# Optimization experiments

Measured on AMD Instinct MI355X. Metric: run time of the kernel, lower is better.

Reference implementation:

```python
import jax, jax.numpy as jnp
import numpy as np

DIM = 1024
HEADS = 16
DIM_HEAD = 64
B = 16
N = 512
INNER = HEADS * DIM_HEAD            # 1024
CPB_DIM = DIM // 2                  # 512
INNER_FF = int(DIM * 4 * 2 / 3)     # 2730
EPS = 1e-5


def setup_inputs() -> dict:
    key = jax.random.key(0)
    ks = jax.random.split(key, 10)
    s = lambda i, shape, scale: jax.random.normal(ks[i], shape, jnp.float32) * scale
    return dict(
        x=s(0, (B, N, DIM), 1.0),
        g_ln=jnp.ones((DIM,), jnp.float32),
        Wq=s(1, (DIM, INNER), 0.02),
        Wkv=s(2, (DIM, 2 * INNER), 0.02),
        Wo=s(3, (INNER, DIM), 0.02),
        cpb_w1=s(4, (1, CPB_DIM), 0.5),
        cpb_b1=jnp.zeros((CPB_DIM,), jnp.float32),
        cpb_w2=s(5, (CPB_DIM, CPB_DIM), 0.05),
        cpb_b2=jnp.zeros((CPB_DIM,), jnp.float32),
        cpb_w3=s(6, (CPB_DIM, HEADS), 0.05),
        cpb_b3=jnp.zeros((HEADS,), jnp.float32),
        ff_w_in=s(7, (2 * INNER_FF, DIM), 0.02),
        ff_g=jnp.ones((INNER_FF,), jnp.float32),
        ff_w_out=s(8, (DIM, INNER_FF), 0.02),
    )


def _seq_ln(x, g):
    # Faithful to repo's LayerNorm: mean/var over dim=1 (sequence axis of [b,n,d])
    mean = jnp.mean(x, axis=1, keepdims=True)
    var = jnp.var(x, axis=1, keepdims=True)  # unbiased=False
    return (x - mean) * jax.lax.rsqrt(jnp.maximum(var, EPS)) * g


def reference(x, g_ln, Wq, Wkv, Wo, cpb_w1, cpb_b1, cpb_w2, cpb_b2, cpb_w3, cpb_b3,
              ff_w_in, ff_g, ff_w_out):
    b, n, d = x.shape
    # ContinuousPositionBias (1D, 2 layers)
    pos = jnp.arange(n, dtype=jnp.float32)
    rel = (pos[:, None] - pos[None, :])[..., None]           # [n,n,1]
    rel = jnp.sign(rel) * jnp.log(jnp.abs(rel) + 1.0)        # log-distance
    h = jax.nn.silu(rel @ cpb_w1 + cpb_b1)
    h = jax.nn.silu(h @ cpb_w2 + cpb_b2)
    bias = (h @ cpb_w3 + cpb_b3).transpose(2, 0, 1)          # [h,n,n]

    # Attention (framerate=None -> no pos_embeds; context = x)
    xn = _seq_ln(x, g_ln)
    q = xn @ Wq
    k, v = jnp.split(xn @ Wkv, 2, axis=-1)
    to_heads = lambda t: t.reshape(b, n, HEADS, DIM_HEAD).transpose(0, 2, 1, 3)
    q, k, v = to_heads(q), to_heads(k), to_heads(v)
    q = q * (DIM_HEAD ** -0.5)
    sim = jnp.einsum('bhid,bhjd->bhij', q, k) + bias[None]
    attn = jax.nn.softmax(sim, axis=-1)
    o = jnp.einsum('bhij,bhjd->bhid', attn, v)
    o = o.transpose(0, 2, 1, 3).reshape(b, n, INNER)
    x = jnp.nan_to_num(o @ Wo) + x

    # FeedForward: Conv1d(k=1) -> GEGLU -> ChanLayerNorm -> Conv1d(k=1), residual
    xt = x.transpose(0, 2, 1)                                # [b,d,n]
    hff = jnp.einsum('oc,bcn->bon', ff_w_in, xt)             # [b,2*inner_ff,n]
    x1, gate = jnp.split(hff, 2, axis=1)
    hff = x1 * jax.nn.gelu(gate, approximate=False)
    mean = jnp.mean(hff, axis=1, keepdims=True)
    var = jnp.var(hff, axis=1, keepdims=True)
    hff = (hff - mean) * jax.lax.rsqrt(jnp.maximum(var, EPS)) * ff_g[None, :, None]
    out = jnp.einsum('oc,bcn->bon', ff_w_out, hff).transpose(0, 2, 1) + x
    return out
```

## Files before the change

### kernel.cpp

```cpp
#include <hip/hip_runtime.h>

#define DEV __device__ __forceinline__

typedef __attribute__((ext_vector_type(8))) short bf16x8;
typedef __attribute__((ext_vector_type(4))) float f32x4;

DEV float b2f(unsigned short u) { union { unsigned int i; float f; } v; v.i = ((unsigned)u) << 16; return v.f; }
DEV unsigned short f2b(float f) {
    union { float f; unsigned int i; } v; v.f = f;
    unsigned r = v.i + 0x7FFFu + ((v.i >> 16) & 1u);
    return (unsigned short)(r >> 16);
}

DEV void llds16(const unsigned short* g, unsigned short* l) {
    __builtin_amdgcn_global_load_lds((const __attribute__((address_space(1))) void*)g,
                                     (__attribute__((address_space(3))) void*)l, 16, 0, 0);
}

DEV float gelu_f(float x) {
    float y = 0.7978845608f * (x + 0.044715f * x * x * x);
    float th = 1.f - 2.f / (__expf(2.f * y) + 1.f);
    return 0.5f * x * (1.f + th);
}

__global__ __launch_bounds__(256) void transpose_cast_k(const float* __restrict__ src,
        unsigned short* __restrict__ dst, int Nc, int K, float scale)
{
    __shared__ float tile[32][33];
    int tx = threadIdx.x, ty = threadIdx.y;
    int c0 = blockIdx.x * 32;
    int r0 = blockIdx.y * 32;
#pragma unroll
    for (int r = 0; r < 4; r++)
        tile[ty + r * 8][tx] = src[(size_t)(r0 + ty + r * 8) * Nc + c0 + tx];
    __syncthreads();
#pragma unroll
    for (int r = 0; r < 4; r++)
        dst[(size_t)(c0 + ty + r * 8) * K + r0 + tx] = f2b(tile[tx][ty + r * 8] * scale);
}

__global__ __launch_bounds__(256) void cast_wfin_k(const float* __restrict__ src,
        unsigned short* __restrict__ dst)
{
    int idx = blockIdx.x * 256 + threadIdx.x;
    int nr = idx >> 8;
    int c4 = (idx & 255) * 4;
    int chunk = nr >> 6, which = (nr >> 5) & 1, pos = nr & 31;
    int c = chunk * 32 + pos;
    unsigned short o0 = 0, o1 = 0, o2 = 0, o3 = 0;
    if (c < 2730) {
        const float* s = src + (size_t)(which * 2730 + c) * 1024 + c4;
        o0 = f2b(s[0]); o1 = f2b(s[1]); o2 = f2b(s[2]); o3 = f2b(s[3]);
    }
    unsigned short* d = dst + (size_t)nr * 1024 + c4;
    d[0] = o0; d[1] = o1; d[2] = o2; d[3] = o3;
}

__global__ __launch_bounds__(256) void cast_wfoutg_k(const float* __restrict__ src,
        const float* __restrict__ g, unsigned short* __restrict__ dst)
{
    int idx = blockIdx.x * 256 + threadIdx.x;
    int r = idx / 2752, c = idx % 2752;
    float v = (c < 2730) ? src[(size_t)r * 2730 + c] * g[c] : 0.f;
    dst[idx] = f2b(v);
}

__global__ __launch_bounds__(64) void wgsum_k(const float* __restrict__ w,
        const float* __restrict__ g, float* __restrict__ wgs)
{
    int o = blockIdx.x, t = threadIdx.x;
    float s = 0.f;
    for (int c = t; c < 2730; c += 64) s += w[(size_t)o * 2730 + c] * g[c];
#pragma unroll
    for (int off = 32; off > 0; off >>= 1) s += __shfl_xor(s, off);
    if (t == 0) wgs[o] = s;
}

__global__ __launch_bounds__(512) void cpb_k(const float* __restrict__ w1, const float* __restrict__ b1,
        const float* __restrict__ w2, const float* __restrict__ b2,
        const float* __restrict__ w3, const float* __restrict__ b3,
        float* __restrict__ btbl)
{
    __shared__ float sH[512];
    __shared__ float sH2[512];
    int t = threadIdx.x, row = blockIdx.x;
    int dd = row - 511;
    float ad = fabsf((float)dd);
    float sgn = (dd > 0) ? 1.f : ((dd < 0) ? -1.f : 0.f);
    float rel = sgn * logf(ad + 1.f);
    float h1 = rel * w1[t] + b1[t];
    h1 = h1 / (1.f + __expf(-h1));
    sH[t] = h1;
    __syncthreads();
    float a = b2[t];
    for (int k = 0; k < 512; k++) a += sH[k] * w2[(size_t)k * 512 + t];
    a = a / (1.f + __expf(-a));
    sH2[t] = a;
    __syncthreads();
    if (t < 16) {
        float s = b3[t];
        for (int k = 0; k < 512; k++) s += sH2[k] * w3[k * 16 + t];
        btbl[t * 1023 + row] = s;
    }
}

__global__ __launch_bounds__(256) void ln_stat_k(const float* __restrict__ x,
        float* __restrict__ part_s, float* __restrict__ part_q)
{
    int b = blockIdx.x >> 4, nc = blockIdx.x & 15, t = threadIdx.x;
    const float* xp = x + ((size_t)b * 512 + nc * 32) * 1024;
#pragma unroll
    for (int dc = 0; dc < 4; dc++) {
        int d = dc * 256 + t;
        float s = 0.f, q = 0.f;
#pragma unroll 8
        for (int n = 0; n < 32; n++) { float v = xp[(size_t)n * 1024 + d]; s += v; q += v * v; }
        part_s[((size_t)b * 16 + nc) * 1024 + d] = s;
        part_q[((size_t)b * 16 + nc) * 1024 + d] = q;
    }
}

__global__ __launch_bounds__(256) void ln_reduce_k(const float* __restrict__ part_s,
        const float* __restrict__ part_q, const float* __restrict__ gln,
        float* __restrict__ mean, float* __restrict__ inv)
{
    int b = blockIdx.x >> 2, d = (blockIdx.x & 3) * 256 + threadIdx.x;
    float s = 0.f, q = 0.f;
#pragma unroll
    for (int c = 0; c < 16; c++) {
        s += part_s[((size_t)b * 16 + c) * 1024 + d];
        q += part_q[((size_t)b * 16 + c) * 1024 + d];
    }
    float m = s * (1.f / 512.f);
    float var = q * (1.f / 512.f) - m * m;
    mean[b * 1024 + d] = m;
    inv[b * 1024 + d] = rsqrtf(fmaxf(var, 1e-5f)) * gln[d];
}

__global__ __launch_bounds__(256) void ln_apply_k(const float* __restrict__ x,
        const float* __restrict__ mean, const float* __restrict__ inv,
        unsigned short* __restrict__ xn)
{
    int b = blockIdx.x >> 4, nc = blockIdx.x & 15, t = threadIdx.x;
    const float* xp = x + ((size_t)b * 512 + nc * 32) * 1024;
    unsigned short* op = xn + ((size_t)b * 512 + nc * 32) * 1024;
#pragma unroll
    for (int dc = 0; dc < 4; dc++) {
        int d = dc * 256 + t;
        float m = mean[b * 1024 + d], iv = inv[b * 1024 + d];
#pragma unroll 8
        for (int n = 0; n < 32; n++)
            op[(size_t)n * 1024 + d] = f2b((xp[(size_t)n * 1024 + d] - m) * iv);
    }
}

__global__ __launch_bounds__(256) void gemm_bt128_k(const unsigned short* __restrict__ A,
        const unsigned short* __restrict__ BT, unsigned short* __restrict__ C,
        float* __restrict__ OUTF, const float* __restrict__ RESF,
        const unsigned short* __restrict__ RESB,
        const float* __restrict__ MU, const float* __restrict__ INVV,
        const float* __restrict__ WGS, int K, int ldc, int mode)
{
    __shared__ __align__(16) unsigned short lds[16384];
    int t = threadIdx.x, lane = t & 63, w = t >> 6;
    int m0 = blockIdx.x * 128, n0 = blockIdx.y * 128;
    int wm = (w >> 1) * 64, wn = (w & 1) * 64;
    int lm = lane & 15, lq = lane >> 4;
    int srow = t >> 2, scol = (t & 3) * 8;
    const unsigned short* gA0 = A + (size_t)(m0 + srow) * K + scol;
    const unsigned short* gB0 = BT + (size_t)(n0 + srow) * K + scol;
    const size_t rstep = (size_t)64 * K;
    int wb = w * 512;

    f32x4 acc[4][4];
#pragma unroll
    for (int i = 0; i < 4; i++)
#pragma unroll
        for (int j = 0; j < 4; j++) acc[i][j] = (f32x4){0.f, 0.f, 0.f, 0.f};

    for (int kk = 0; kk < K; kk += 64) {
        __syncthreads();
        llds16(gA0 + kk,              &lds[wb]);
        llds16(gA0 + rstep + kk,      &lds[2048 + wb]);
        llds16(gB0 + kk,              &lds[4096 + wb]);
        llds16(gB0 + rstep + kk,      &lds[6144 + wb]);
        llds16(gA0 + kk + 32,         &lds[8192 + wb]);
        llds16(gA0 + rstep + kk + 32, &lds[10240 + wb]);
        llds16(gB0 + kk + 32,         &lds[12288 + wb]);
        llds16(gB0 + rstep + kk + 32, &lds[14336 + wb]);
        __syncthreads();
#pragma unroll
        for (int p = 0; p < 2; p++) {
            int pa = p * 8192, pb = p * 8192 + 4096;
            bf16x8 af[4], bfr[4];
#pragma unroll
            for (int i = 0; i < 4; i++) af[i] = *(const bf16x8*)&lds[pa + (wm + i * 16 + lm) * 32 + lq * 8];
#pragma unroll
            for (int j = 0; j < 4; j++) bfr[j] = *(const bf16x8*)&lds[pb + (wn + j * 16 + lm) * 32 + lq * 8];
#pragma unroll
            for (int i = 0; i < 4; i++)
#pragma unroll
                for (int j = 0; j < 4; j++)
                    acc[i][j] = __builtin_amdgcn_mfma_f32_16x16x32_bf16(af[i], bfr[j], acc[i][j], 0, 0, 0);
        }
    }

#pragma unroll
    for (int i = 0; i < 4; i++)
#pragma unroll
        for (int j = 0; j < 4; j++)
#pragma unroll
            for (int r = 0; r < 4; r++) {
                int row = m0 + wm + i * 16 + lq * 4 + r;
                int col = n0 + wn + j * 16 + lm;
                size_t idx = (size_t)row * ldc + col;
                float v = acc[i][j][r];
                if (mode == 1) { v += RESF[idx]; C[idx] = f2b(v); }
                if (mode == 2) {
                    float iv = INVV[row];
                    v = v * iv - MU[row] * iv * WGS[col] + b2f(RESB[idx]);
                    OUTF[idx] = v;
                }
            }
}


#define RDA8(AF, MH, BUF) { \
    _Pragma("unroll") \
    for (int i_ = 0; i_ < 4; i_++) { \
        AF[i_][0] = *(const bf16x8*)(sc8 + (BUF) + rbA + (MH) * 8192 + i_ * 2048 + soff0); \
        AF[i_][1] = *(const bf16x8*)(sc8 + (BUF) + rbA + (MH) * 8192 + i_ * 2048 + soff1); \
    } }
#define RDB8(BF, NH, BUF) { \
    _Pragma("unroll") \
    for (int j_ = 0; j_ < 2; j_++) { \
        BF[j_][0] = *(const bf16x8*)(sc8 + (BUF) + 32768 + rbB + (NH) * 4096 + j_ * 2048 + soff0); \
        BF[j_][1] = *(const bf16x8*)(sc8 + (BUF) + 32768 + rbB + (NH) * 4096 + j_ * 2048 + soff1); \
    } }
#define MFQ8(MH, NH, AF, BF) { \
    __builtin_amdgcn_s_setprio(1); \
    _Pragma("unroll") \
    for (int i_ = 0; i_ < 4; i_++) { \
        _Pragma("unroll") \
        for (int j_ = 0; j_ < 2; j_++) { \
            acc[(MH) * 4 + i_][(NH) * 2 + j_] = __builtin_amdgcn_mfma_f32_16x16x32_bf16( \
                AF[i_][0], BF[j_][0], acc[(MH) * 4 + i_][(NH) * 2 + j_], 0, 0, 0); \
            acc[(MH) * 4 + i_][(NH) * 2 + j_] = __builtin_amdgcn_mfma_f32_16x16x32_bf16( \
                AF[i_][1], BF[j_][1], acc[(MH) * 4 + i_][(NH) * 2 + j_], 0, 0, 0); \
        } } \
    __builtin_amdgcn_s_setprio(0); }
#define STGA8(BUF, H, KE) do { \
    llds16(A + oA[(H) * 2] + (KE),     &sL[((BUF) + (H) * 16384 + wst) >> 1]); \
    llds16(A + oA[(H) * 2 + 1] + (KE), &sL[((BUF) + (H) * 16384 + 8192 + wst) >> 1]); \
} while (0)
#define STGB8(BUF, H, KE) do { \
    llds16(BT + oB[(H) * 2] + (KE),     &sL[((BUF) + 32768 + (H) * 16384 + wst) >> 1]); \
    llds16(BT + oB[(H) * 2 + 1] + (KE), &sL[((BUF) + 32768 + (H) * 16384 + 8192 + wst) >> 1]); \
} while (0)
#define TILE6(TTV, DO_A, DO_B2, LASTW) { \
    int bufc_ = ((TTV) & 1) << 16; \
    int bufn_ = bufc_ ^ 65536; \
    int kA1_ = ((TTV) + 1) * 64; \
    int kB2_ = ((TTV) + 2) * 64; \
    (void)bufn_; (void)kA1_; (void)kB2_; \
    bf16x8 a0[4][2], a1[4][2], b0[2][2], b1[2][2]; \
    RDA8(a0, 0, bufc_); \
    RDB8(b0, 0, bufc_); \
    if (DO_A) STGA8(bufn_, 0, kA1_); \
    MFQ8(0, 0, a0, b0); \
    __builtin_amdgcn_s_barrier(); \
    RDB8(b1, 1, bufc_); \
    if (DO_A) STGA8(bufn_, 1, kA1_); \
    MFQ8(0, 1, a0, b1); \
    __builtin_amdgcn_s_barrier(); \
    RDA8(a1, 1, bufc_); \
    if (DO_B2) STGB8(bufc_, 0, kB2_); \
    MFQ8(1, 0, a1, b0); \
    if (DO_B2) STGB8(bufc_, 1, kB2_); \
    MFQ8(1, 1, a1, b1); \
    if ((LASTW) == 4) asm volatile("s_waitcnt vmcnt(4)" ::: "memory"); \
    if ((LASTW) == 0) asm volatile("s_waitcnt vmcnt(0)" ::: "memory"); \
    __builtin_amdgcn_s_barrier(); \
}

template<int MODE, int NTILES>
__global__ __launch_bounds__(512, 2) void g8_k(const unsigned short* __restrict__ A,
        const unsigned short* __restrict__ BT, unsigned short* __restrict__ OUT,
        int NB, int ldc)
{
    __shared__ __align__(16) unsigned short sL[65536];
    const char* sc8 = (const char*)sL;
    int t = threadIdx.x, lane = t & 63, w = t >> 6;
    int bid = blockIdx.x;
    int m0 = ((bid & 7) * 4 + ((bid >> 3) & 3)) * 256;
    int n0 = (bid >> 5) * 256;
    int wm = (w >> 2) * 128, wn = (w & 3) * 64;
    int lm = lane & 15, lq = lane >> 4;
    int rbA = wm * 128, rbB = wn * 128;
    int soff0 = lm * 128 + ((lq ^ (lm & 7)) << 4);
    int soff1 = lm * 128 + (((4 | lq) ^ (lm & 7)) << 4);
    int wst = w * 1024;
    int sr = t >> 3;
    int scw = ((t & 7) ^ (sr & 7)) << 3;
    int oA[4], oB[4];
#pragma unroll
    for (int hp = 0; hp < 4; hp++) {
        oA[hp] = (m0 + hp * 64 + sr) * 1024 + scw;
        int rb = n0 + hp * 64 + sr;
        if (rb > NB - 1) rb = NB - 1;
        oB[hp] = rb * 1024 + scw;
    }

    f32x4 acc[8][4];
#pragma unroll
    for (int i = 0; i < 8; i++)
#pragma unroll
        for (int j = 0; j < 4; j++) acc[i][j] = (f32x4){0.f, 0.f, 0.f, 0.f};

    STGB8(0, 0, 0);
    STGB8(0, 1, 0);
    STGA8(0, 0, 0);
    STGA8(0, 1, 0);
    STGB8(65536, 0, 64);
    STGB8(65536, 1, 64);
    asm volatile("s_waitcnt vmcnt(4)" ::: "memory");
    __builtin_amdgcn_s_barrier();

#pragma unroll 2
    for (int tt = 0; tt < NTILES - 2; tt++) TILE6(tt, 1, 1, 4);
    TILE6(NTILES - 2, 1, 0, 0);
    TILE6(NTILES - 1, 0, 0, -1);

    if (MODE == 0) {
#pragma unroll
        for (int i = 0; i < 8; i++)
#pragma unroll
            for (int j = 0; j < 4; j++)
#pragma unroll
                for (int r = 0; r < 4; r++) {
                    int row = m0 + wm + i * 16 + lq * 4 + r;
                    int col = n0 + wn + j * 16 + lm;
                    OUT[(size_t)row * ldc + col] = f2b(acc[i][j][r]);
                }
    } else {
        int chunk = (n0 + wn) >> 6;
        if (chunk < 86) {
#pragma unroll
            for (int i = 0; i < 8; i++)
#pragma unroll
                for (int jp = 0; jp < 2; jp++)
#pragma unroll
                    for (int r = 0; r < 4; r++) {
                        int row = m0 + wm + i * 16 + lq * 4 + r;
                        int c = chunk * 32 + jp * 16 + lm;
                        OUT[(size_t)row * 2752 + c] = f2b(acc[i][jp][r] * gelu_f(acc[i][jp + 2][r]));
                    }
        }
    }
}

#undef RDA8
#undef RDB8
#undef MFQ8
#undef STGA8
#undef STGB8
#undef TILE6

__global__ __launch_bounds__(256) void vtrans_k(const unsigned short* __restrict__ qkv,
        unsigned short* __restrict__ vT)
{
    __shared__ unsigned short sT[64 * 72];
    int t = threadIdx.x;
    int jt = blockIdx.x, bh = blockIdx.y;
    int b = bh >> 4, h = bh & 15;
#pragma unroll
    for (int it = 0; it < 16; it++) {
        int idx = it * 256 + t;
        int jl = idx >> 6, d = idx & 63;
        sT[d * 72 + jl] = qkv[((size_t)(b * 512 + jt * 64 + jl)) * 3072 + 2048 + h * 64 + d];
    }
    __syncthreads();
#pragma unroll
    for (int it = 0; it < 16; it++) {
        int idx = it * 256 + t;
        int d = idx >> 6, jl = idx & 63;
        vT[((size_t)(bh * 64 + d)) * 512 + jt * 64 + jl] = sT[d * 72 + jl];
    }
}

__global__ __launch_bounds__(256) void attn_k(const unsigned short* __restrict__ qkv,
        const unsigned short* __restrict__ vT, const float* __restrict__ btbl,
        unsigned short* __restrict__ attno)
{
    __shared__ __align__(16) unsigned short sQ[8192];
    __shared__ __align__(16) unsigned short sK[8192];
    __shared__ __align__(16) unsigned short sVT[8192];
    __shared__ __align__(16) unsigned short sP[8192];
    __shared__ float sB[1024];
    int t = threadIdx.x, lane = t & 63, w = t >> 6;
    int qt = blockIdx.x, h = blockIdx.y, b = blockIdx.z;
    int lm = lane & 15, lq = lane >> 4;
    int bh = b * 16 + h;
    int lrow4 = lane >> 2, lch = lane & 3;

    for (int i = t; i < 1023; i += 256) sB[i] = btbl[h * 1023 + i];

#pragma unroll
    for (int c = 0; c < 4; c++) {
        int cidx = w * 4 + c;
        int panel = cidx >> 3, r0 = (cidx & 7) * 16;
        const unsigned short* g = qkv + ((size_t)(b * 512 + qt * 128 + r0 + lrow4)) * 3072
                                  + h * 64 + panel * 32 + lch * 8;
        llds16(g, &sQ[panel * 4096 + r0 * 32]);
    }

    f32x4 o[2][4];
    float lrow[2][4];
#pragma unroll
    for (int it = 0; it < 2; it++)
#pragma unroll
        for (int z = 0; z < 4; z++) o[it][z] = (f32x4){0.f, 0.f, 0.f, 0.f};
#pragma unroll
    for (int it = 0; it < 2; it++)
#pragma unroll
        for (int r = 0; r < 4; r++) lrow[it][r] = 0.f;

    __syncthreads();

    bf16x8 aq[2][2];
#pragma unroll
    for (int it = 0; it < 2; it++)
#pragma unroll
        for (int kh = 0; kh < 2; kh++)
            aq[it][kh] = *(const bf16x8*)&sQ[kh * 4096 + (w * 32 + it * 16 + lm) * 32 + lq * 8];

    for (int jj = 0; jj < 4; jj++) {
        __syncthreads();
#pragma unroll
        for (int c = 0; c < 4; c++) {
            int cidx = w * 4 + c;
            int panel = cidx >> 3, r0 = (cidx & 7) * 16;
            const unsigned short* g = qkv + ((size_t)(b * 512 + jj * 128 + r0 + lrow4)) * 3072
                                      + 1024 + h * 64 + panel * 32 + lch * 8;
            llds16(g, &sK[panel * 4096 + r0 * 32]);
        }
#pragma unroll
        for (int c = 0; c < 4; c++) {
            int cidx = w * 4 + c;
            int panel = cidx >> 2, d0 = (cidx & 3) * 16;
            const unsigned short* g = vT + ((size_t)(bh * 64 + d0 + lrow4)) * 512
                                      + jj * 128 + panel * 32 + lch * 8;
            llds16(g, &sVT[panel * 2048 + d0 * 32]);
        }
        __syncthreads();

#pragma unroll
        for (int ch2 = 0; ch2 < 2; ch2++) {
            f32x4 s[2][4];
#pragma unroll
            for (int it = 0; it < 2; it++)
#pragma unroll
                for (int jt = 0; jt < 4; jt++) {
                    int jl = ch2 * 64 + jt * 16 + lm;
                    f32x4 c0 = {0.f, 0.f, 0.f, 0.f};
                    c0 = __builtin_amdgcn_mfma_f32_16x16x32_bf16(aq[it][0],
                            *(const bf16x8*)&sK[jl * 32 + lq * 8], c0, 0, 0, 0);
                    c0 = __builtin_amdgcn_mfma_f32_16x16x32_bf16(aq[it][1],
                            *(const bf16x8*)&sK[4096 + jl * 32 + lq * 8], c0, 0, 0, 0);
                    s[it][jt] = c0;
                }
            int jbase = jj * 128 + ch2 * 64;
#pragma unroll
            for (int it = 0; it < 2; it++) {
                int ibase = qt * 128 + w * 32 + it * 16;
#pragma unroll
                for (int r = 0; r < 4; r++) {
                    int ip = ibase + lq * 4 + r + 511 - jbase - lm;
                    float p0 = __expf(s[it][0][r] + sB[ip]);
                    float p1 = __expf(s[it][1][r] + sB[ip - 16]);
                    float p2 = __expf(s[it][2][r] + sB[ip - 32]);
                    float p3 = __expf(s[it][3][r] + sB[ip - 48]);
                    lrow[it][r] += (p0 + p1) + (p2 + p3);
                    int rowl = it * 16 + lq * 4 + r;
                    unsigned short* pp = &sP[w * 2048 + rowl * 64 + lm];
                    pp[0]  = f2b(p0);
                    pp[16] = f2b(p1);
                    pp[32] = f2b(p2);
                    pp[48] = f2b(p3);
                }
            }
#pragma unroll
            for (int it = 0; it < 2; it++)
#pragma unroll
                for (int kh = 0; kh < 2; kh++) {
                    bf16x8 ap = *(const bf16x8*)&sP[w * 2048 + (it * 16 + lm) * 64 + kh * 32 + lq * 8];
#pragma unroll
                    for (int dt = 0; dt < 4; dt++) {
                        bf16x8 bv = *(const bf16x8*)&sVT[(ch2 * 2 + kh) * 2048 + (dt * 16 + lm) * 32 + lq * 8];
                        o[it][dt] = __builtin_amdgcn_mfma_f32_16x16x32_bf16(ap, bv, o[it][dt], 0, 0, 0);
                    }
                }
        }
    }

#pragma unroll
    for (int it = 0; it < 2; it++)
#pragma unroll
        for (int r = 0; r < 4; r++) {
            float tot = lrow[it][r];
#pragma unroll
            for (int off = 8; off > 0; off >>= 1) tot += __shfl_xor(tot, off);
            float inv = 1.f / tot;
            int row = b * 512 + qt * 128 + w * 32 + it * 16 + lq * 4 + r;
#pragma unroll
            for (int dt = 0; dt < 4; dt++)
                attno[(size_t)row * 1024 + h * 64 + dt * 16 + lm] = f2b(o[it][dt][r] * inv);
        }
}

__global__ __launch_bounds__(256) void chstat_k(const unsigned short* __restrict__ hffg,
        float* __restrict__ mu, float* __restrict__ inv)
{
    int row = blockIdx.x, t = threadIdx.x;
    const unsigned short* rp = hffg + (size_t)row * 2752;
    float sum = 0.f, ss = 0.f;
    for (int v8 = t; v8 < 344; v8 += 256) {
        bf16x8 x = *(const bf16x8*)&rp[v8 * 8];
#pragma unroll
        for (int e = 0; e < 8; e++) {
            float f = b2f((unsigned short)x[e]);
            sum += f; ss += f * f;
        }
    }
#pragma unroll
    for (int off = 32; off > 0; off >>= 1) { sum += __shfl_xor(sum, off); ss += __shfl_xor(ss, off); }
    __shared__ float rb[8];
    int w = t >> 6;
    if ((t & 63) == 0) { rb[w] = sum; rb[4 + w] = ss; }
    __syncthreads();
    if (t == 0) {
        sum = rb[0] + rb[1] + rb[2] + rb[3];
        ss = rb[4] + rb[5] + rb[6] + rb[7];
        float m = sum * (1.f / 2730.f);
        float var = ss * (1.f / 2730.f) - m * m;
        mu[row] = m;
        inv[row] = rsqrtf(fmaxf(var, 1e-5f));
    }
}

extern "C" void kernel_launch(void* const* d_in, const int* in_sizes, int n_in,
                              void* d_out, int out_size, void* d_ws, size_t ws_size,
                              hipStream_t stream) {
    const float* x      = (const float*)d_in[0];
    const float* g_ln   = (const float*)d_in[1];
    const float* Wq     = (const float*)d_in[2];
    const float* Wkv    = (const float*)d_in[3];
    const float* Wo     = (const float*)d_in[4];
    const float* cw1    = (const float*)d_in[5];
    const float* cb1    = (const float*)d_in[6];
    const float* cw2    = (const float*)d_in[7];
    const float* cb2    = (const float*)d_in[8];
    const float* cw3    = (const float*)d_in[9];
    const float* cb3    = (const float*)d_in[10];
    const float* ffwin  = (const float*)d_in[11];
    const float* ffg    = (const float*)d_in[12];
    const float* ffwout = (const float*)d_in[13];

    char* ws = (char*)d_ws;
    unsigned short* xn    = (unsigned short*)(ws + 0);
    unsigned short* wqkvT = (unsigned short*)(ws + 16777216);
    unsigned short* woT   = (unsigned short*)(ws + 23068672);
    unsigned short* qkv   = (unsigned short*)(ws + 25165824);
    unsigned short* vT    = (unsigned short*)(ws + 75497472);
    unsigned short* attno = (unsigned short*)(ws + 92274688);
    unsigned short* hffg  = (unsigned short*)(ws + 0);
    unsigned short* wfin  = (unsigned short*)(ws + 109051904);
    unsigned short* wfout = (unsigned short*)(ws + 120324096);
    float*          btbl  = (float*)(ws + 125960192);
    unsigned short* x2b   = (unsigned short*)(ws + 126025728);
    float*          part_s = (float*)(ws + 142802944);
    float*          part_q = (float*)(ws + 143851520);
    float*          lnmean = (float*)(ws + 144900096);
    float*          lninv  = (float*)(ws + 144965632);
    float*          chmu   = (float*)(ws + 145031168);
    float*          chinv  = (float*)(ws + 145063936);
    float*          wgs    = (float*)(ws + 145096704);

    dim3 tb(32, 8);
    transpose_cast_k<<<dim3(32, 32), tb, 0, stream>>>(Wq, wqkvT, 1024, 1024, 0.125f);
    transpose_cast_k<<<dim3(64, 32), tb, 0, stream>>>(Wkv, wqkvT + (size_t)1024 * 1024, 2048, 1024, 1.0f);
    transpose_cast_k<<<dim3(32, 32), tb, 0, stream>>>(Wo, woT, 1024, 1024, 1.0f);
    cast_wfin_k<<<5504, 256, 0, stream>>>(ffwin, wfin);
    cast_wfoutg_k<<<11008, 256, 0, stream>>>(ffwout, ffg, wfout);
    wgsum_k<<<1024, 64, 0, stream>>>(ffwout, ffg, wgs);
    cpb_k<<<1023, 512, 0, stream>>>(cw1, cb1, cw2, cb2, cw3, cb3, btbl);
    ln_stat_k<<<256, 256, 0, stream>>>(x, part_s, part_q);
    ln_reduce_k<<<64, 256, 0, stream>>>(part_s, part_q, g_ln, lnmean, lninv);
    ln_apply_k<<<256, 256, 0, stream>>>(x, lnmean, lninv, xn);
    g8_k<0, 16><<<dim3(384), 512, 0, stream>>>(xn, wqkvT, qkv, 3072, 3072);
    vtrans_k<<<dim3(8, 256), 256, 0, stream>>>(qkv, vT);
    attn_k<<<dim3(4, 16, 16), 256, 0, stream>>>(qkv, vT, btbl, attno);
    gemm_bt128_k<<<dim3(64, 8), 256, 0, stream>>>(attno, woT, x2b, nullptr, x, nullptr,
                                                  nullptr, nullptr, nullptr, 1024, 1024, 1);
    g8_k<1, 16><<<dim3(704), 512, 0, stream>>>(x2b, wfin, hffg, 5504, 0);
    chstat_k<<<8192, 256, 0, stream>>>(hffg, chmu, chinv);
    gemm_bt128_k<<<dim3(64, 8), 256, 0, stream>>>(hffg, wfout, nullptr, (float*)d_out, nullptr, x2b,
                                                  chmu, chinv, wgs, 2752, 1024, 2);
}
```

Baseline: 590.5 us.

## Replace simple 128x128 GEMM with pipelined 256x128 swizzled double-buffered kernel

Replaces the Wo projection and FF output GEMMs with a new 512-thread kernel that computes 256x128 tiles. It double-buffers LDS with staggered A/B prefetch via global_load_lds and swizzles the LDS layout to avoid bank conflicts. It also interleaves MFMA with staging under explicit vmcnt waits and remaps block indices for L2 locality. The aim is to hide global-load latency and cut the sync stalls of the old single-buffered loop. The cost is more LDS per block and a hardcoded ldc of 1024 and tile counts.

After: 520.2 us. 11.9% less time.

```diff
diff --git a/kernel.cpp b/kernel.cpp
--- a/kernel.cpp
+++ b/kernel.cpp
@@ -152,76 +152,6 @@
         for (int n = 0; n < 32; n++)
             op[(size_t)n * 1024 + d] = f2b((xp[(size_t)n * 1024 + d] - m) * iv);
     }
-}
-
-__global__ __launch_bounds__(256) void gemm_bt128_k(const unsigned short* __restrict__ A,
-        const unsigned short* __restrict__ BT, unsigned short* __restrict__ C,
-        float* __restrict__ OUTF, const float* __restrict__ RESF,
-        const unsigned short* __restrict__ RESB,
-        const float* __restrict__ MU, const float* __restrict__ INVV,
-        const float* __restrict__ WGS, int K, int ldc, int mode)
-{
-    __shared__ __align__(16) unsigned short lds[16384];
-    int t = threadIdx.x, lane = t & 63, w = t >> 6;
-    int m0 = blockIdx.x * 128, n0 = blockIdx.y * 128;
-    int wm = (w >> 1) * 64, wn = (w & 1) * 64;
-    int lm = lane & 15, lq = lane >> 4;
-    int srow = t >> 2, scol = (t & 3) * 8;
-    const unsigned short* gA0 = A + (size_t)(m0 + srow) * K + scol;
-    const unsigned short* gB0 = BT + (size_t)(n0 + srow) * K + scol;
-    const size_t rstep = (size_t)64 * K;
-    int wb = w * 512;
-
-    f32x4 acc[4][4];
-#pragma unroll
-    for (int i = 0; i < 4; i++)
-#pragma unroll
-        for (int j = 0; j < 4; j++) acc[i][j] = (f32x4){0.f, 0.f, 0.f, 0.f};
-
-    for (int kk = 0; kk < K; kk += 64) {
-        __syncthreads();
-        llds16(gA0 + kk,              &lds[wb]);
-        llds16(gA0 + rstep + kk,      &lds[2048 + wb]);
-        llds16(gB0 + kk,              &lds[4096 + wb]);
-        llds16(gB0 + rstep + kk,      &lds[6144 + wb]);
-        llds16(gA0 + kk + 32,         &lds[8192 + wb]);
-        llds16(gA0 + rstep + kk + 32, &lds[10240 + wb]);
-        llds16(gB0 + kk + 32,         &lds[12288 + wb]);
-        llds16(gB0 + rstep + kk + 32, &lds[14336 + wb]);
-        __syncthreads();
-#pragma unroll
-        for (int p = 0; p < 2; p++) {
-            int pa = p * 8192, pb = p * 8192 + 4096;
-            bf16x8 af[4], bfr[4];
-#pragma unroll
-            for (int i = 0; i < 4; i++) af[i] = *(const bf16x8*)&lds[pa + (wm + i * 16 + lm) * 32 + lq * 8];
-#pragma unroll
-            for (int j = 0; j < 4; j++) bfr[j] = *(const bf16x8*)&lds[pb + (wn + j * 16 + lm) * 32 + lq * 8];
-#pragma unroll
-            for (int i = 0; i < 4; i++)
-#pragma unroll
-                for (int j = 0; j < 4; j++)
-                    acc[i][j] = __builtin_amdgcn_mfma_f32_16x16x32_bf16(af[i], bfr[j], acc[i][j], 0, 0, 0);
-        }
-    }
-
-#pragma unroll
-    for (int i = 0; i < 4; i++)
-#pragma unroll
-        for (int j = 0; j < 4; j++)
-#pragma unroll
-            for (int r = 0; r < 4; r++) {
-                int row = m0 + wm + i * 16 + lq * 4 + r;
-                int col = n0 + wn + j * 16 + lm;
-                size_t idx = (size_t)row * ldc + col;
-                float v = acc[i][j][r];
-                if (mode == 1) { v += RESF[idx]; C[idx] = f2b(v); }
-                if (mode == 2) {
-                    float iv = INVV[row];
-                    v = v * iv - MU[row] * iv * WGS[col] + b2f(RESB[idx]);
-                    OUTF[idx] = v;
-                }
-            }
 }
 
 
@@ -366,6 +296,138 @@
 #undef STGB8
 #undef TILE6
 
+
+#define GRDA(AF, MH, BUF) { \
+    _Pragma("unroll") \
+    for (int i_ = 0; i_ < 2; i_++) { \
+        AF[i_][0] = *(const bf16x8*)(sc8 + (BUF) + rbA + (MH) * 4096 + i_ * 2048 + soff0); \
+        AF[i_][1] = *(const bf16x8*)(sc8 + (BUF) + rbA + (MH) * 4096 + i_ * 2048 + soff1); \
+    } }
+#define GRDB(BF, NH, BUF) { \
+    _Pragma("unroll") \
+    for (int j_ = 0; j_ < 2; j_++) { \
+        BF[j_][0] = *(const bf16x8*)(sc8 + (BUF) + 32768 + rbB + (NH) * 4096 + j_ * 2048 + soff0); \
+        BF[j_][1] = *(const bf16x8*)(sc8 + (BUF) + 32768 + rbB + (NH) * 4096 + j_ * 2048 + soff1); \
+    } }
+#define GMFQ(MH, NH, AF, BF) { \
+    __builtin_amdgcn_s_setprio(1); \
+    _Pragma("unroll") \
+    for (int i_ = 0; i_ < 2; i_++) { \
+        _Pragma("unroll") \
+        for (int j_ = 0; j_ < 2; j_++) { \
+            acc[(MH) * 2 + i_][(NH) * 2 + j_] = __builtin_amdgcn_mfma_f32_16x16x32_bf16( \
+                AF[i_][0], BF[j_][0], acc[(MH) * 2 + i_][(NH) * 2 + j_], 0, 0, 0); \
+            acc[(MH) * 2 + i_][(NH) * 2 + j_] = __builtin_amdgcn_mfma_f32_16x16x32_bf16( \
+                AF[i_][1], BF[j_][1], acc[(MH) * 2 + i_][(NH) * 2 + j_], 0, 0, 0); \
+        } } \
+    __builtin_amdgcn_s_setprio(0); }
+#define GSTGA(BUF, H, KE) do { \
+    llds16(A + oA[(H) * 2] + (KE),     &sL[((BUF) + (H) * 16384 + wst) >> 1]); \
+    llds16(A + oA[(H) * 2 + 1] + (KE), &sL[((BUF) + (H) * 16384 + 8192 + wst) >> 1]); \
+} while (0)
+#define GSTGB(BUF, C_, KE) \
+    llds16(BT + oB[C_] + (KE), &sL[((BUF) + 32768 + (C_) * 8192 + wst) >> 1])
+#define GTILE(TTV, DO_A, DO_B2, LASTW) { \
+    int bufc_ = ((TTV) & 1) * 49152; \
+    int bufn_ = 49152 - bufc_; \
+    int kA1_ = ((TTV) + 1) * 64; \
+    int kB2_ = ((TTV) + 2) * 64; \
+    (void)bufn_; (void)kA1_; (void)kB2_; \
+    bf16x8 a0[2][2], a1[2][2], b0[2][2], b1[2][2]; \
+    GRDA(a0, 0, bufc_); \
+    GRDB(b0, 0, bufc_); \
+    if (DO_A) GSTGA(bufn_, 0, kA1_); \
+    GMFQ(0, 0, a0, b0); \
+    __builtin_amdgcn_s_barrier(); \
+    GRDB(b1, 1, bufc_); \
+    if (DO_A) GSTGA(bufn_, 1, kA1_); \
+    GMFQ(0, 1, a0, b1); \
+    __builtin_amdgcn_s_barrier(); \
+    GRDA(a1, 1, bufc_); \
+    if (DO_B2) GSTGB(bufc_, 0, kB2_); \
+    GMFQ(1, 0, a1, b0); \
+    if (DO_B2) GSTGB(bufc_, 1, kB2_); \
+    GMFQ(1, 1, a1, b1); \
+    if ((LASTW) == 2) asm volatile("s_waitcnt vmcnt(2)" ::: "memory"); \
+    if ((LASTW) == 0) asm volatile("s_waitcnt vmcnt(0)" ::: "memory"); \
+    __builtin_amdgcn_s_barrier(); \
+}
+
+template<int MODE, int NT>
+__global__ __launch_bounds__(512, 2) void g128_k(const unsigned short* __restrict__ A,
+        const unsigned short* __restrict__ BT, unsigned short* __restrict__ C,
+        float* __restrict__ OUTF, const float* __restrict__ RESF,
+        const unsigned short* __restrict__ RESB,
+        const float* __restrict__ MU, const float* __restrict__ INVV,
+        const float* __restrict__ WGS, int K)
+{
+    __shared__ __align__(16) unsigned short sL[49152];
+    const char* sc8 = (const char*)sL;
+    int t = threadIdx.x, lane = t & 63, w = t >> 6;
+    int bid = blockIdx.x;
+    int m0 = ((bid & 7) * 4 + ((bid >> 3) & 3)) * 256;
+    int n0 = (bid >> 5) * 128;
+    int wm = (w >> 1) * 64, wn = (w & 1) * 64;
+    int lm = lane & 15, lq = lane >> 4;
+    int rbA = wm * 128, rbB = wn * 128;
+    int soff0 = lm * 128 + ((lq ^ (lm & 7)) << 4);
+    int soff1 = lm * 128 + (((4 | lq) ^ (lm & 7)) << 4);
+    int wst = w * 1024;
+    int sr = t >> 3;
+    int scw = ((t & 7) ^ (sr & 7)) << 3;
+    int oA[4], oB[2];
+#pragma unroll
+    for (int hp = 0; hp < 4; hp++)
+        oA[hp] = (m0 + (hp >> 1) * 128 + (hp & 1) * 64 + sr) * K + scw;
+#pragma unroll
+    for (int c = 0; c < 2; c++)
+        oB[c] = (n0 + c * 64 + sr) * K + scw;
+
+    f32x4 acc[4][4];
+#pragma unroll
+    for (int i = 0; i < 4; i++)
+#pragma unroll
+        for (int j = 0; j < 4; j++) acc[i][j] = (f32x4){0.f, 0.f, 0.f, 0.f};
+
+    GSTGB(0, 0, 0);
+    GSTGB(0, 1, 0);
+    GSTGA(0, 0, 0);
+    GSTGA(0, 1, 0);
+    GSTGB(49152, 0, 64);
+    GSTGB(49152, 1, 64);
+    asm volatile("s_waitcnt vmcnt(2)" ::: "memory");
+    __builtin_amdgcn_s_barrier();
+
+    for (int tt = 0; tt < NT - 2; tt++) GTILE(tt, 1, 1, 2);
+    GTILE(NT - 2, 1, 0, 0);
+    GTILE(NT - 1, 0, 0, -1);
+
+#pragma unroll
+    for (int i = 0; i < 4; i++)
+#pragma unroll
+        for (int j = 0; j < 4; j++)
+#pragma unroll
+            for (int r = 0; r < 4; r++) {
+                int row = m0 + wm + i * 16 + lq * 4 + r;
+                int col = n0 + wn + j * 16 + lm;
+                size_t idx = (size_t)row * 1024 + col;
+                float v = acc[i][j][r];
+                if (MODE == 1) { v += RESF[idx]; C[idx] = f2b(v); }
+                if (MODE == 2) {
+                    float iv = INVV[row];
+                    v = v * iv - MU[row] * iv * WGS[col] + b2f(RESB[idx]);
+                    OUTF[idx] = v;
+                }
+            }
+}
+
+#undef GRDA
+#undef GRDB
+#undef GMFQ
+#undef GSTGA
+#undef GSTGB
+#undef GTILE
+
 __global__ __launch_bounds__(256) void vtrans_k(const unsigned short* __restrict__ qkv,
         unsigned short* __restrict__ vT)
 {
@@ -600,10 +662,10 @@
     g8_k<0, 16><<<dim3(384), 512, 0, stream>>>(xn, wqkvT, qkv, 3072, 3072);
     vtrans_k<<<dim3(8, 256), 256, 0, stream>>>(qkv, vT);
     attn_k<<<dim3(4, 16, 16), 256, 0, stream>>>(qkv, vT, btbl, attno);
-    gemm_bt128_k<<<dim3(64, 8), 256, 0, stream>>>(attno, woT, x2b, nullptr, x, nullptr,
-                                                  nullptr, nullptr, nullptr, 1024, 1024, 1);
+    g128_k<1, 16><<<dim3(256), 512, 0, stream>>>(attno, woT, x2b, nullptr, x, nullptr,
+                                                 nullptr, nullptr, nullptr, 1024);
     g8_k<1, 16><<<dim3(704), 512, 0, stream>>>(x2b, wfin, hffg, 5504, 0);
     chstat_k<<<8192, 256, 0, stream>>>(hffg, chmu, chinv);
-    gemm_bt128_k<<<dim3(64, 8), 256, 0, stream>>>(hffg, wfout, nullptr, (float*)d_out, nullptr, x2b,
-                                                  chmu, chinv, wgs, 2752, 1024, 2);
-}
+    g128_k<2, 43><<<dim3(256), 512, 0, stream>>>(hffg, wfout, nullptr, (float*)d_out, nullptr, x2b,
+                                                 chmu, chinv, wgs, 2752);
+}
```
